# Performance work log

Measured on AMD Instinct MI355X. Metric: run time of the kernel, lower is better.

The kernel has to match this reference:

```python
import jax, jax.numpy as jnp
import numpy as np

N = 65536        # nodes
E = 131072       # directed edges
D = 512          # emb_dim
L = 5            # num_layer
G = 512          # num graphs
EPS = 1e-5       # batchnorm eps
NUM_ATOM_TYPE, NUM_CHIRALITY = 120, 3
NUM_BOND_TYPE, NUM_BOND_DIR = 6, 3


def setup_inputs() -> dict:
    key = jax.random.key(0)
    ks = jax.random.split(key, 12)
    s = 0.02
    return {
        "x": jax.random.randint(ks[0], (N, 2), 0, 3),
        "edge_index": jax.random.randint(ks[1], (2, E), 0, N),
        "edge_attr": jax.random.randint(ks[2], (E, 2), 0, 3),
        "batch": jnp.sort(jax.random.randint(ks[3], (N,), 0, G)),
        "x_emb1": jax.random.normal(ks[4], (NUM_ATOM_TYPE, D), jnp.float32) * s,
        "x_emb2": jax.random.normal(ks[5], (NUM_CHIRALITY, D), jnp.float32) * s,
        "e_emb1": jax.random.normal(ks[6], (L, NUM_BOND_TYPE, D), jnp.float32) * s,
        "e_emb2": jax.random.normal(ks[7], (L, NUM_BOND_DIR, D), jnp.float32) * s,
        "W1": jax.random.normal(ks[8], (L, D, 2 * D), jnp.float32) * s,
        "b1": jnp.zeros((L, 2 * D), jnp.float32),
        "W2": jax.random.normal(ks[9], (L, 2 * D, D), jnp.float32) * s,
        "b2": jnp.zeros((L, D), jnp.float32),
        "gamma": jnp.ones((L, D), jnp.float32),
        "beta": jnp.zeros((L, D), jnp.float32),
    }


def reference(x, edge_index, edge_attr, batch,
              x_emb1, x_emb2, e_emb1, e_emb2,
              W1, b1, W2, b2, gamma, beta):
    n = x.shape[0]
    # atom embedding: type + chirality
    h = x_emb1[x[:, 0]] + x_emb2[x[:, 1]]                     # [N, D]

    # add self loops (appended after real edges, attr = [4, 0])
    loops = jnp.arange(n)
    src = jnp.concatenate([edge_index[0], loops])             # [E+N]
    dst = jnp.concatenate([edge_index[1], loops])
    sl_attr = jnp.concatenate(
        [jnp.full((n, 1), 4, dtype=edge_attr.dtype),
         jnp.zeros((n, 1), dtype=edge_attr.dtype)], axis=1)
    ea = jnp.concatenate([edge_attr, sl_attr], axis=0)        # [E+N, 2]

    for l in range(L):
        # per-edge embedding: bond type + bond direction
        e = e_emb1[l][ea[:, 0]] + e_emb2[l][ea[:, 1]]         # [E+N, D]
        msg = h[src] + e                                      # gather + add
        agg = jax.ops.segment_sum(msg, dst, num_segments=n)   # scatter-add
        # GIN MLP: Linear(D,2D) -> ReLU -> Linear(2D,D)
        hh = jax.nn.relu(agg @ W1[l] + b1[l]) @ W2[l] + b2[l]
        # BatchNorm1d (training-mode batch statistics)
        mean = hh.mean(axis=0)
        var = hh.var(axis=0)
        hh = (hh - mean) * jax.lax.rsqrt(var + EPS) * gamma[l] + beta[l]
        if l < L - 1:
            hh = jax.nn.relu(hh)   # dropout(p=0) is identity
        h = hh

    # JK='last': node rep = h; graph rep = global mean pool over batch ids
    counts = jax.ops.segment_sum(jnp.ones((n,), h.dtype), batch, num_segments=G)
    graph = jax.ops.segment_sum(h, batch, num_segments=G) / jnp.maximum(counts, 1.0)[:, None]
    return graph, h
```

## Files before the change

kernel.cpp:

```cpp
#include <hip/hip_runtime.h>
#include <stdint.h>

#define Nn 65536
#define Ee 131072
#define Dd 512
#define D2 1024
#define Ll 5
#define Gg 512
#define EPSf 1e-5f

typedef _Float16 f16x8 __attribute__((ext_vector_type(8)));
typedef float f32x4 __attribute__((ext_vector_type(4)));
typedef unsigned short u16x8 __attribute__((ext_vector_type(8)));

__device__ __forceinline__ unsigned short f2h(float f) {
    _Float16 h = (_Float16)f;
    union { _Float16 h; unsigned short u; } c; c.h = h;
    return c.u;
}

__device__ __forceinline__ float4 h4f(ushort4 u) {
    union { unsigned short s; _Float16 h; } a, b, c, d;
    a.s = u.x; b.s = u.y; c.s = u.z; d.s = u.w;
    return make_float4((float)a.h, (float)b.h, (float)c.h, (float)d.h);
}

__device__ __forceinline__ void add4(float4& a, float4 b) {
    a.x += b.x; a.y += b.y; a.z += b.z; a.w += b.w;
}

__device__ __forceinline__ void gload_lds16(const void* g, void* l) {
    __builtin_amdgcn_global_load_lds(
        (const __attribute__((address_space(1))) void*)(uintptr_t)g,
        (__attribute__((address_space(3))) void*)(unsigned)(uintptr_t)l,
        16, 0, 0);
}

__global__ void k_transW(const float* __restrict__ src, unsigned short* __restrict__ dst,
                         int K, int Nw) {
    long total = (long)Ll * K * Nw;
    for (long idx = (long)blockIdx.x * blockDim.x + threadIdx.x; idx < total;
         idx += (long)gridDim.x * blockDim.x) {
        long l = idx / ((long)K * Nw);
        long rem = idx - l * (long)K * Nw;
        int k = (int)(rem / Nw), n = (int)(rem % Nw);
        dst[(l * Nw + n) * K + k] = f2h(src[idx]);
    }
}

__global__ void k_embed(const int* __restrict__ x,
                        const float4* __restrict__ xe1, const float4* __restrict__ xe2,
                        float4* __restrict__ h4) {
    const int total = Nn * 128;
    for (int idx = blockIdx.x * blockDim.x + threadIdx.x; idx < total;
         idx += gridDim.x * blockDim.x) {
        int node = idx >> 7, c = idx & 127;
        int t0 = x[2 * node], t1 = x[2 * node + 1];
        float4 v = xe1[t0 * 128 + c];
        float4 w = xe2[t1 * 128 + c];
        v.x += w.x; v.y += w.y; v.z += w.z; v.w += w.w;
        h4[idx] = v;
    }
}

__global__ void k_zeroN(int* __restrict__ p, int n) {
    int i = blockIdx.x * blockDim.x + threadIdx.x;
    if (i < n) p[i] = 0;
}

__global__ void k_hist(const int* __restrict__ edst, int* __restrict__ cnt) {
    int e = blockIdx.x * blockDim.x + threadIdx.x;
    if (e < Ee) atomicAdd(&cnt[edst[e]], 1);
}

__global__ void k_scan(const int* __restrict__ cnt, int* __restrict__ off,
                       int* __restrict__ cursor) {
    __shared__ int part[1024];
    int t = threadIdx.x;
    int base = t * 64;
    int s = 0;
    for (int i = 0; i < 64; ++i) s += cnt[base + i];
    part[t] = s;
    __syncthreads();
    for (int d = 1; d < 1024; d <<= 1) {
        int v = (t >= d) ? part[t - d] : 0;
        __syncthreads();
        part[t] += v;
        __syncthreads();
    }
    int run = part[t] - s;
    for (int i = 0; i < 64; ++i) {
        off[base + i] = run;
        cursor[base + i] = run;
        run += cnt[base + i];
    }
    if (t == 1023) off[Nn] = run;
}

__global__ void k_place(const int* __restrict__ esrc, const int* __restrict__ edst,
                        const int* __restrict__ eattr, int* __restrict__ cursor,
                        int* __restrict__ ckey, int* __restrict__ csrc) {
    int e = blockIdx.x * blockDim.x + threadIdx.x;
    if (e < Ee) {
        int d = edst[e];
        int p = atomicAdd(&cursor[d], 1);
        ckey[p] = e * 32 + (eattr[2 * e] * 3 + eattr[2 * e + 1]);
        csrc[p] = esrc[e];
    }
}

__global__ void k_sort(const int* __restrict__ off, int* __restrict__ ckey,
                       int* __restrict__ csrc) {
    int node = blockIdx.x * blockDim.x + threadIdx.x;
    if (node >= Nn) return;
    int kb = off[node], ke = off[node + 1];
    for (int i = kb + 1; i < ke; ++i) {
        int k = ckey[i], s = csrc[i];
        int j = i - 1;
        while (j >= kb && ckey[j] > k) {
            ckey[j + 1] = ckey[j]; csrc[j + 1] = csrc[j]; --j;
        }
        ckey[j + 1] = k; csrc[j + 1] = s;
    }
}

template <int NORM>
__global__ __launch_bounds__(256) void k_gather(const float* __restrict__ hf32,
                                                const unsigned short* __restrict__ hf16,
                                                const float* __restrict__ ss,
                                                const int* __restrict__ off,
                                                const int* __restrict__ ckey,
                                                const int* __restrict__ csrc,
                                                const float* __restrict__ e1l,
                                                const float* __restrict__ e2l,
                                                unsigned short* __restrict__ aggh) {
    int node = (blockIdx.x << 2) + (threadIdx.x >> 6);
    int lane = threadIdx.x & 63;
    int c0 = lane, c1 = lane + 64;
    float4 sa0, sb0, sa1, sb1;
    if (NORM) {
        const float4* ss4 = (const float4*)ss;
        sa0 = ss4[c0]; sb0 = ss4[128 + c0];
        sa1 = ss4[c1]; sb1 = ss4[128 + c1];
    }
    auto loadrow = [&](size_t rowbase, int c, float4 a, float4 b) -> float4 {
        float4 v;
        if (NORM) {
            v = h4f(*(const ushort4*)(hf16 + rowbase + (size_t)c * 4));
            v.x = fmaxf(fmaf(v.x, a.x, b.x), 0.f);
            v.y = fmaxf(fmaf(v.y, a.y, b.y), 0.f);
            v.z = fmaxf(fmaf(v.z, a.z, b.z), 0.f);
            v.w = fmaxf(fmaf(v.w, a.w, b.w), 0.f);
        } else {
            v = *(const float4*)(hf32 + rowbase + (size_t)c * 4);
        }
        return v;
    };
    const float4* s1 = (const float4*)(e1l + 4 * Dd);
    const float4* s2 = (const float4*)(e2l);
    size_t nb = (size_t)node * Dd;
    float4 A0 = loadrow(nb, c0, sa0, sb0);
    float4 A1 = loadrow(nb, c1, sa1, sb1);
    add4(A0, s1[c0]); add4(A0, s2[c0]);
    add4(A1, s1[c1]); add4(A1, s2[c1]);
    int kb = off[node], ke = off[node + 1];
    for (int k = kb; k < ke; ++k) {
        size_t sb = (size_t)csrc[k] * Dd;
        int at = ckey[k] & 31;
        const float4* p1 = (const float4*)(e1l + (size_t)(at / 3) * Dd);
        const float4* p2 = (const float4*)(e2l + (size_t)(at % 3) * Dd);
        add4(A0, loadrow(sb, c0, sa0, sb0)); add4(A0, p1[c0]); add4(A0, p2[c0]);
        add4(A1, loadrow(sb, c1, sa1, sb1)); add4(A1, p1[c1]); add4(A1, p2[c1]);
    }
    unsigned short* dst = aggh + (size_t)node * Dd;
    ushort4 o0, o1;
    o0.x = f2h(A0.x); o0.y = f2h(A0.y); o0.z = f2h(A0.z); o0.w = f2h(A0.w);
    o1.x = f2h(A1.x); o1.y = f2h(A1.y); o1.z = f2h(A1.z); o1.w = f2h(A1.w);
    *(ushort4*)(dst + c0 * 4) = o0;
    *(ushort4*)(dst + c1 * 4) = o1;
}

__device__ __forceinline__ void stage_q(const unsigned short* __restrict__ g, int ldk,
                                        long row0, int col0, char* region, int tid) {
    int wbase = (tid >> 6) << 10;
#pragma unroll
    for (int r = 0; r < 2; ++r) {
        int gi = tid + r * 512;
        int row = gi >> 2;
        int k16 = (gi & 3) ^ ((row >> 1) & 3);
        gload_lds16(g + (row0 + row) * (long)ldk + col0 + k16 * 8,
                    region + r * 8192 + wbase);
    }
}

__device__ __forceinline__ f16x8 rd_frag(const char* region, int row, int l4) {
    int slot = l4 ^ ((row >> 1) & 3);
    return *(const f16x8*)(region + row * 64 + (slot << 4));
}

template <int EPI>
__global__ __launch_bounds__(512, 2) void gemm8(const unsigned short* __restrict__ A,
                                                const unsigned short* __restrict__ BT,
                                                const float* __restrict__ bias,
                                                unsigned short* __restrict__ Cb,
                                                float* __restrict__ pS,
                                                int M, int N, int K) {
    __shared__ __align__(16) char lds[65536];
    const int tid = threadIdx.x;
    const int lane = tid & 63;
    const int w = tid >> 6;
    const int wm = w >> 2, wn = w & 3;
    const int l15 = lane & 15, l4 = lane >> 4;

    const int nwg = gridDim.x;
    const int cpx = nwg >> 3;
    const int bid = blockIdx.x;
    const int wg = (bid & 7) * cpx + (bid >> 3);
    const int ntn = N >> 8;
    const long bm = (long)(wg / ntn) * 256;
    const long bn = (long)(wg % ntn) * 256;

    char* Ar = lds;
    char* Br = lds + 32768;
    const int NT = K >> 5;

    f32x4 acc[8][4];
#pragma unroll
    for (int i = 0; i < 8; ++i)
#pragma unroll
        for (int j = 0; j < 4; ++j) acc[i][j] = (f32x4){0.f, 0.f, 0.f, 0.f};

    stage_q(A, K, bm, 0, Ar, tid);
    stage_q(BT, K, bn, 0, Br, tid);
    asm volatile("s_waitcnt vmcnt(0)" ::: "memory");
    __builtin_amdgcn_s_barrier();

    for (int t = 0; t < NT; ++t) {
        const char* Ac = Ar + (t & 1) * 16384;
        const char* Bc = Br + (t & 1) * 16384;
        if (t + 1 < NT) {
            stage_q(A, K, bm, (t + 1) * 32, Ar + ((t + 1) & 1) * 16384, tid);
            stage_q(BT, K, bn, (t + 1) * 32, Br + ((t + 1) & 1) * 16384, tid);
        }
        f16x8 af[8], bv[4];
#pragma unroll
        for (int fm = 0; fm < 8; ++fm)
            af[fm] = rd_frag(Ac, wm * 128 + fm * 16 + l15, l4);
#pragma unroll
        for (int fn = 0; fn < 4; ++fn)
            bv[fn] = rd_frag(Bc, wn * 64 + fn * 16 + l15, l4);
        __builtin_amdgcn_s_barrier();
        asm volatile("s_waitcnt lgkmcnt(0)" ::: "memory");
        __builtin_amdgcn_s_setprio(1);
#pragma unroll
        for (int fm = 0; fm < 8; ++fm)
#pragma unroll
            for (int fn = 0; fn < 4; ++fn)
                acc[fm][fn] = __builtin_amdgcn_mfma_f32_16x16x32_f16(af[fm], bv[fn], acc[fm][fn], 0, 0, 0);
        __builtin_amdgcn_s_setprio(0);
        if (t + 1 < NT) {
            asm volatile("s_waitcnt vmcnt(0)" ::: "memory");
        }
        __builtin_amdgcn_s_barrier();
    }

    unsigned short* cl = (unsigned short*)lds;
    float cs[4] = {0.f, 0.f, 0.f, 0.f}, cq[4] = {0.f, 0.f, 0.f, 0.f};
#pragma unroll
    for (int q = 0; q < 4; ++q) {
        __syncthreads();
        if (wm == (q >> 1)) {
#pragma unroll
            for (int fn = 0; fn < 4; ++fn) {
                int col = wn * 64 + fn * 16 + l15;
                float bval = bias[bn + col];
#pragma unroll
                for (int fi = 0; fi < 4; ++fi) {
                    const int fm = (q & 1) * 4 + fi;
                    int rl = fi * 16 + l4 * 4;
#pragma unroll
                    for (int r = 0; r < 4; ++r) {
                        float v = acc[fm][fn][r] + bval;
                        if (EPI == 0) v = fmaxf(v, 0.f);
                        else { cs[fn] += v; cq[fn] += v * v; }
                        cl[(rl + r) * 264 + col] = f2h(v);
                    }
                }
            }
        }
        __syncthreads();
#pragma unroll
        for (int i = 0; i < 4; ++i) {
            int g = tid + i * 512;
            int r = g >> 5, cg = (g & 31) << 3;
            u16x8 val = *(const u16x8*)&cl[r * 264 + cg];
            *(u16x8*)&Cb[(bm + q * 64 + r) * N + bn + cg] = val;
        }
    }
    if (EPI == 1) {
#pragma unroll
        for (int fn = 0; fn < 4; ++fn) {
            float s = cs[fn], q = cq[fn];
            s += __shfl_xor(s, 16); s += __shfl_xor(s, 32);
            q += __shfl_xor(q, 16); q += __shfl_xor(q, 32);
            if (l4 == 0) {
                int col = (int)bn + wn * 64 + fn * 16 + l15;
                int rowgrp = ((int)(bm >> 8)) * 2 + wm;
                pS[rowgrp * 512 + col] = s;
                pS[262144 + rowgrp * 512 + col] = q;
            }
        }
    }
}

__global__ void k_bnred(const float* __restrict__ pS, const float* __restrict__ gamma,
                        const float* __restrict__ beta, float* __restrict__ ss) {
    int col = blockIdx.x * 256 + threadIdx.x;
    float s = 0.f, q = 0.f;
    for (int rg = 0; rg < 512; ++rg) {
        s += pS[rg * 512 + col];
        q += pS[262144 + rg * 512 + col];
    }
    float mean = s * (1.f / (float)Nn);
    float var = q * (1.f / (float)Nn) - mean * mean;
    float a = gamma[col] * rsqrtf(var + EPSf);
    ss[col] = a;
    ss[512 + col] = beta[col] - mean * a;
}

__global__ void k_norm(const unsigned short* __restrict__ hhf, const float* __restrict__ ss,
                       float4* __restrict__ h4) {
    const int total = Nn * 128;
    const float4* ss4 = (const float4*)ss;
    for (int idx = blockIdx.x * blockDim.x + threadIdx.x; idx < total;
         idx += gridDim.x * blockDim.x) {
        int c = idx & 127;
        float4 v = h4f(*(const ushort4*)(hhf + (size_t)idx * 4));
        float4 a = ss4[c], b = ss4[128 + c];
        v.x = fmaf(v.x, a.x, b.x); v.y = fmaf(v.y, a.y, b.y);
        v.z = fmaf(v.z, a.z, b.z); v.w = fmaf(v.w, a.w, b.w);
        h4[idx] = v;
    }
}

__global__ void k_pool(const unsigned short* __restrict__ hhf, const float* __restrict__ ss,
                       const int* __restrict__ batch, float* __restrict__ graph) {
    int g = blockIdx.x, t = threadIdx.x;
    int lo = 0, hi = Nn;
    while (lo < hi) { int m = (lo + hi) >> 1; if (batch[m] < g) lo = m + 1; else hi = m; }
    int s = lo;
    lo = s; hi = Nn;
    while (lo < hi) { int m = (lo + hi) >> 1; if (batch[m] <= g) lo = m + 1; else hi = m; }
    int e = lo;
    float a0 = ss[t], a1 = ss[t + 256];
    float b0 = ss[512 + t], b1 = ss[512 + t + 256];
    union { unsigned short s; _Float16 h; } u0, u1;
    float s0 = 0.f, s1 = 0.f;
    for (int r = s; r < e; ++r) {
        const unsigned short* row = hhf + (size_t)r * Dd;
        u0.s = row[t]; u1.s = row[t + 256];
        s0 += fmaf((float)u0.h, a0, b0);
        s1 += fmaf((float)u1.h, a1, b1);
    }
    int cnt = e - s; if (cnt < 1) cnt = 1;
    float inv = 1.f / (float)cnt;
    graph[(long)g * Dd + t] = s0 * inv;
    graph[(long)g * Dd + t + 256] = s1 * inv;
}

extern "C" void kernel_launch(void* const* d_in, const int* in_sizes, int n_in,
                              void* d_out, int out_size, void* d_ws, size_t ws_size,
                              hipStream_t stream) {
    (void)in_sizes; (void)n_in; (void)out_size; (void)ws_size;
    const int* x      = (const int*)d_in[0];
    const int* ei     = (const int*)d_in[1];
    const int* ea     = (const int*)d_in[2];
    const int* batch  = (const int*)d_in[3];
    const float* xe1  = (const float*)d_in[4];
    const float* xe2  = (const float*)d_in[5];
    const float* ee1  = (const float*)d_in[6];
    const float* ee2  = (const float*)d_in[7];
    const float* W1   = (const float*)d_in[8];
    const float* b1   = (const float*)d_in[9];
    const float* W2   = (const float*)d_in[10];
    const float* b2   = (const float*)d_in[11];
    const float* gamma = (const float*)d_in[12];
    const float* beta  = (const float*)d_in[13];

    float* graph = (float*)d_out;
    float* h = graph + (size_t)Gg * Dd;

    char* w = (char*)d_ws;
    int* csr_off = (int*)w;                     w += (Nn + 1) * 4;
    int* cursor = (int*)w;                      w += Nn * 4;
    int* cnt = (int*)w;                         w += Nn * 4;
    int* ckey = (int*)w;                        w += Ee * 4;
    int* csrc = (int*)w;                        w += Ee * 4;
    float* ss = (float*)w;                      w += 4096;
    float* pS = (float*)w;                      w += 2 * 512 * 512 * 4;
    unsigned short* aggh = (unsigned short*)w;  w += (size_t)Nn * Dd * 2;
    unsigned short* hhf = (unsigned short*)w;   w += (size_t)Nn * Dd * 2;
    unsigned short* w1t = (unsigned short*)w;   w += (size_t)Ll * D2 * Dd * 2;
    unsigned short* w2t = (unsigned short*)w;   w += (size_t)Ll * Dd * D2 * 2;

    k_transW<<<2048, 256, 0, stream>>>(W1, w1t, Dd, D2);
    k_transW<<<2048, 256, 0, stream>>>(W2, w2t, D2, Dd);

    k_embed<<<2048, 256, 0, stream>>>(x, (const float4*)xe1, (const float4*)xe2, (float4*)h);

    k_zeroN<<<64, 1024, 0, stream>>>(cnt, Nn);
    k_hist<<<Ee / 256, 256, 0, stream>>>(ei + Ee, cnt);
    k_scan<<<1, 1024, 0, stream>>>(cnt, csr_off, cursor);
    k_place<<<Ee / 256, 256, 0, stream>>>(ei, ei + Ee, ea, cursor, ckey, csrc);
    k_sort<<<Nn / 256, 256, 0, stream>>>(csr_off, ckey, csrc);

    for (int l = 0; l < Ll; ++l) {
        const float* e1l = ee1 + (size_t)l * 6 * Dd;
        const float* e2l = ee2 + (size_t)l * 3 * Dd;
        if (l == 0)
            k_gather<0><<<Nn / 4, 256, 0, stream>>>(h, nullptr, nullptr, csr_off, ckey, csrc,
                                                    e1l, e2l, aggh);
        else
            k_gather<1><<<Nn / 4, 256, 0, stream>>>(nullptr, hhf, ss, csr_off, ckey, csrc,
                                                    e1l, e2l, aggh);
        gemm8<0><<<(Nn / 256) * (D2 / 256), 512, 0, stream>>>(
            aggh, w1t + (size_t)l * D2 * Dd, b1 + (size_t)l * D2,
            (unsigned short*)h, nullptr, Nn, D2, Dd);
        gemm8<1><<<(Nn / 256) * (Dd / 256), 512, 0, stream>>>(
            (const unsigned short*)h, w2t + (size_t)l * Dd * D2, b2 + (size_t)l * Dd,
            hhf, pS, Nn, Dd, D2);
        k_bnred<<<2, 256, 0, stream>>>(pS, gamma + (size_t)l * Dd, beta + (size_t)l * Dd, ss);
    }

    k_norm<<<2048, 256, 0, stream>>>(hhf, ss, (float4*)h);
    k_pool<<<Gg, 256, 0, stream>>>(hhf, ss, batch, graph);
}
```

Baseline: 1.678 ms.

## Deepen GEMM K-tile to 64 with split-half prefetch and fewer barriers

The GEMM main loop now stages 64-wide K tiles in two 32-wide halves, double-buffered across 128KB of LDS. Each half's prefetch is issued after its fragments are read and is waited on with a partial vmcnt, so global loads overlap MFMA work across halves. The epilogue also writes 128-row chunks in two passes instead of 64-row chunks in four, cutting synchronisations. The larger LDS footprint means only one 512-thread workgroup fits per CU, despite launch_bounds requesting two, which reduces occupancy and latency hiding.

```diff
diff --git a/kernel.cpp b/kernel.cpp
--- a/kernel.cpp
+++ b/kernel.cpp
@@ -205,7 +205,7 @@
                                                 unsigned short* __restrict__ Cb,
                                                 float* __restrict__ pS,
                                                 int M, int N, int K) {
-    __shared__ __align__(16) char lds[65536];
+    __shared__ __align__(16) char lds[131072];
     const int tid = threadIdx.x;
     const int lane = tid & 63;
     const int w = tid >> 6;
@@ -221,8 +221,8 @@
     const long bn = (long)(wg % ntn) * 256;
 
     char* Ar = lds;
-    char* Br = lds + 32768;
-    const int NT = K >> 5;
+    char* Br = lds + 65536;
+    const int NT = K >> 6;
 
     f32x4 acc[8][4];
 #pragma unroll
@@ -232,69 +232,76 @@
 
     stage_q(A, K, bm, 0, Ar, tid);
     stage_q(BT, K, bn, 0, Br, tid);
-    asm volatile("s_waitcnt vmcnt(0)" ::: "memory");
+    stage_q(A, K, bm, 32, Ar + 16384, tid);
+    stage_q(BT, K, bn, 32, Br + 16384, tid);
+    asm volatile("s_waitcnt vmcnt(4)" ::: "memory");
     __builtin_amdgcn_s_barrier();
+    asm volatile("" ::: "memory");
 
     for (int t = 0; t < NT; ++t) {
-        const char* Ac = Ar + (t & 1) * 16384;
-        const char* Bc = Br + (t & 1) * 16384;
-        if (t + 1 < NT) {
-            stage_q(A, K, bm, (t + 1) * 32, Ar + ((t + 1) & 1) * 16384, tid);
-            stage_q(BT, K, bn, (t + 1) * 32, Br + ((t + 1) & 1) * 16384, tid);
-        }
-        f16x8 af[8], bv[4];
-#pragma unroll
-        for (int fm = 0; fm < 8; ++fm)
-            af[fm] = rd_frag(Ac, wm * 128 + fm * 16 + l15, l4);
-#pragma unroll
-        for (int fn = 0; fn < 4; ++fn)
-            bv[fn] = rd_frag(Bc, wn * 64 + fn * 16 + l15, l4);
-        __builtin_amdgcn_s_barrier();
-        asm volatile("s_waitcnt lgkmcnt(0)" ::: "memory");
-        __builtin_amdgcn_s_setprio(1);
-#pragma unroll
-        for (int fm = 0; fm < 8; ++fm)
+        const int par = (t & 1) << 15;
+        const int npar = ((t + 1) & 1) << 15;
+        const bool pre = (t + 1 < NT);
+#pragma unroll
+        for (int kh = 0; kh < 2; ++kh) {
+            const char* Ac = Ar + par + kh * 16384;
+            const char* Bc = Br + par + kh * 16384;
+            f16x8 af[8], bv[4];
 #pragma unroll
             for (int fn = 0; fn < 4; ++fn)
-                acc[fm][fn] = __builtin_amdgcn_mfma_f32_16x16x32_f16(af[fm], bv[fn], acc[fm][fn], 0, 0, 0);
-        __builtin_amdgcn_s_setprio(0);
-        if (t + 1 < NT) {
-            asm volatile("s_waitcnt vmcnt(0)" ::: "memory");
-        }
-        __builtin_amdgcn_s_barrier();
+                bv[fn] = rd_frag(Bc, wn * 64 + fn * 16 + l15, l4);
+#pragma unroll
+            for (int fm = 0; fm < 8; ++fm)
+                af[fm] = rd_frag(Ac, wm * 128 + fm * 16 + l15, l4);
+            if (pre) {
+                stage_q(BT, K, bn, (t + 1) * 64 + kh * 32, Br + npar + kh * 16384, tid);
+                stage_q(A, K, bm, (t + 1) * 64 + kh * 32, Ar + npar + kh * 16384, tid);
+            }
+#pragma unroll
+            for (int fm = 0; fm < 8; ++fm)
+#pragma unroll
+                for (int fn = 0; fn < 4; ++fn)
+                    acc[fm][fn] = __builtin_amdgcn_mfma_f32_16x16x32_f16(af[fm], bv[fn], acc[fm][fn], 0, 0, 0);
+            if (pre) {
+                asm volatile("s_waitcnt vmcnt(4)" ::: "memory");
+            } else {
+                asm volatile("s_waitcnt vmcnt(0)" ::: "memory");
+            }
+            __builtin_amdgcn_s_barrier();
+            asm volatile("" ::: "memory");
+        }
     }
 
     unsigned short* cl = (unsigned short*)lds;
     float cs[4] = {0.f, 0.f, 0.f, 0.f}, cq[4] = {0.f, 0.f, 0.f, 0.f};
 #pragma unroll
-    for (int q = 0; q < 4; ++q) {
+    for (int hh = 0; hh < 2; ++hh) {
         __syncthreads();
-        if (wm == (q >> 1)) {
+        if (wm == hh) {
 #pragma unroll
             for (int fn = 0; fn < 4; ++fn) {
                 int col = wn * 64 + fn * 16 + l15;
                 float bval = bias[bn + col];
 #pragma unroll
-                for (int fi = 0; fi < 4; ++fi) {
-                    const int fm = (q & 1) * 4 + fi;
-                    int rl = fi * 16 + l4 * 4;
+                for (int fm = 0; fm < 8; ++fm) {
+                    int r0 = fm * 16 + l4 * 4;
 #pragma unroll
                     for (int r = 0; r < 4; ++r) {
                         float v = acc[fm][fn][r] + bval;
                         if (EPI == 0) v = fmaxf(v, 0.f);
                         else { cs[fn] += v; cq[fn] += v * v; }
-                        cl[(rl + r) * 264 + col] = f2h(v);
+                        cl[(r0 + r) * 264 + col] = f2h(v);
                     }
                 }
             }
         }
         __syncthreads();
 #pragma unroll
-        for (int i = 0; i < 4; ++i) {
+        for (int i = 0; i < 8; ++i) {
             int g = tid + i * 512;
             int r = g >> 5, cg = (g & 31) << 3;
             u16x8 val = *(const u16x8*)&cl[r * 264 + cg];
-            *(u16x8*)&Cb[(bm + q * 64 + r) * N + bn + cg] = val;
+            *(u16x8*)&Cb[(bm + hh * 128 + r) * N + bn + cg] = val;
         }
     }
     if (EPI == 1) {
```

New measurement: 1.622 ms. 1.03x faster.
